# Performance work log

Measured on AMD Instinct MI355X. Metric: run time of the kernel, lower is better.

Reference implementation:

```python
import jax, jax.numpy as jnp
import numpy as np

B, N, F, U, S = 64, 4096, 2, 16, 2


def setup_inputs() -> dict:
    key = jax.random.key(0)
    ks = jax.random.split(key, 7)
    inputs = jax.random.normal(ks[0], (B, F * N), dtype=jnp.float32)
    state = jax.random.normal(ks[1], (B, U * N), dtype=jnp.float32)

    def random_walk(k):
        a = jax.random.uniform(k, (N, N), dtype=jnp.float32)
        return a / jnp.sum(a, axis=1, keepdims=True)  # row-stochastic like D^-1 A

    support0 = random_walk(ks[2])
    support1 = random_walk(ks[3])
    kshape = ((F + U) * S, U)
    scale = jnp.float32(1.0 / np.sqrt(kshape[0]))
    r_kernel = jax.random.normal(ks[4], kshape, dtype=jnp.float32) * scale
    u_kernel = jax.random.normal(ks[5], kshape, dtype=jnp.float32) * scale
    c_kernel = jax.random.normal(ks[6], kshape, dtype=jnp.float32) * scale
    return {"inputs": inputs, "state": state, "support0": support0,
            "support1": support1, "r_kernel": r_kernel, "u_kernel": u_kernel,
            "c_kernel": c_kernel}


def _diffuse(x, supports):
    # x: (B, C, N); K.dot(x, support.T)[b,c,m] = sum_n x[b,c,n] * support[m,n]
    return jnp.concatenate([jnp.einsum('bcn,mn->bcm', x, s) for s in supports], axis=1)


def reference(inputs, state, support0, support1, r_kernel, u_kernel, c_kernel):
    supports = (support0, support1)
    feats = inputs.reshape(B, F, N)
    prev = state.reshape(B, U, N)

    h = _diffuse(feats, supports).transpose(0, 2, 1)   # (B, N, S*F)
    st = _diffuse(prev, supports).transpose(0, 2, 1)   # (B, N, S*U)
    hs = jnp.concatenate([h, st], axis=-1)             # (B, N, S*(F+U))

    r = jax.nn.sigmoid(hs @ r_kernel)                  # (B, N, U)
    u = jax.nn.sigmoid(hs @ u_kernel)                  # (B, N, U)

    prev_t = prev.transpose(0, 2, 1)                   # (B, N, U)
    r_prev = (r * prev_t).transpose(0, 2, 1)           # (B, U, N)
    c_state = _diffuse(r_prev, supports).transpose(0, 2, 1)  # (B, N, S*U)
    c = jnp.tanh(jnp.concatenate([h, c_state], axis=-1) @ c_kernel)  # (B, N, U)

    z = u * prev_t + (1.0 - u) * c                     # (B, N, U)
    # original: activation=None -> linear, then K.reshape(output, (-1, units*num_nodes))
    return z.reshape(B, U * N)
```

## Files before the change

kernel.cpp:

```cpp
#include <hip/hip_runtime.h>
#include <cstdint>

#define KDIM 4096
#define NNODE 4096
#define KSPLIT 2
#define TSTEPS 128
#define THALF (TSTEPS / KSPLIT)

typedef __bf16 bf16x8 __attribute__((ext_vector_type(8)));
typedef float floatx4 __attribute__((ext_vector_type(4)));

__device__ __forceinline__ uint16_t f2b(float f) {
  union { float f; uint32_t u; } v; v.f = f;
  uint32_t u = v.u;
  return (uint16_t)((u + 0x7FFFu + ((u >> 16) & 1u)) >> 16);
}
__device__ __forceinline__ float b2f(uint16_t h) {
  union { uint32_t u; float f; } v; v.u = ((uint32_t)h) << 16; return v.f;
}
__device__ __forceinline__ uint32_t pack2(float a, float b) {
  return (uint32_t)f2b(a) | ((uint32_t)f2b(b) << 16);
}


__global__ __launch_bounds__(256) void cvt_supports(
    const float* __restrict__ s0, const float* __restrict__ s1,
    uint16_t* __restrict__ d0, uint16_t* __restrict__ d1) {
  const float* src = blockIdx.z ? s1 : s0;
  uint16_t* dst = blockIdx.z ? d1 : d0;
  const int c16 = blockIdx.x, kb = blockIdx.y;
  const int col_in = threadIdx.x >> 4, k8 = threadIdx.x & 15;
  const int col = c16 * 16 + col_in;
  const int k = kb * 128 + k8 * 8;
  const float* p = src + (size_t)col * KDIM + k;
  float4 v0 = *(const float4*)p;
  float4 v1 = *(const float4*)(p + 4);
  uint4 o;
  o.x = pack2(v0.x, v0.y); o.y = pack2(v0.z, v0.w);
  o.z = pack2(v1.x, v1.y); o.w = pack2(v1.z, v1.w);
  size_t off = ((size_t)(c16 * 128 + kb * 4 + (k8 >> 2))) * 512 +
               (size_t)((k8 & 3) * 16 + col_in) * 8;
  *(uint4*)(dst + off) = o;
}

__global__ __launch_bounds__(256) void pack_x1(
    const float* __restrict__ inp, const float* __restrict__ st,
    uint16_t* __restrict__ X1) {
  const int r16 = blockIdx.x, kb = blockIdx.y;
  const int row_in = threadIdx.x >> 4, k8 = threadIdx.x & 15;
  const int row = r16 * 16 + row_in;
  const int k = kb * 128 + k8 * 8;
  int b = row / 18, c = row - b * 18;
  const float* p = (c < 2) ? (inp + (size_t)b * 8192 + (size_t)c * 4096 + k)
                           : (st + (size_t)b * 65536 + (size_t)(c - 2) * 4096 + k);
  float4 v0 = *(const float4*)p;
  float4 v1 = *(const float4*)(p + 4);
  uint4 o;
  o.x = pack2(v0.x, v0.y); o.y = pack2(v0.z, v0.w);
  o.z = pack2(v1.x, v1.y); o.w = pack2(v1.z, v1.w);
  size_t off = ((size_t)(r16 * 128 + kb * 4 + (k8 >> 2))) * 512 +
               (size_t)((k8 & 3) * 16 + row_in) * 8;
  *(uint4*)(X1 + off) = o;
}

__device__ __forceinline__ void gl_lds16(const uint16_t* g, uint16_t* l) {
  __builtin_amdgcn_global_load_lds(
      (const __attribute__((address_space(1))) uint32_t*)g,
      (__attribute__((address_space(3))) uint32_t*)l, 16, 0, 0);
}

template <int MODE>
__global__ __launch_bounds__(256) void gemm_frag(
    const uint16_t* __restrict__ Af, const uint16_t* __restrict__ S0f,
    const uint16_t* __restrict__ S1f, uint16_t* __restrict__ D) {
  constexpr int CPB = (MODE == 1) ? 18 : 16;
  constexpr int OUTC = (MODE == 1) ? 36 : 32;
  constexpr size_t PSTRIDE = (size_t)64 * OUTC * NNODE;
  constexpr int KCH = THALF / 2;

  __shared__ uint16_t sAB[2][32][512];

  const int lane = threadIdx.x & 63, wave = threadIdx.x >> 6;
  const int wr = wave >> 1, wc = wave & 1;
  const int s = blockIdx.z & 1, ks = blockIdx.z >> 1;
  const uint16_t* __restrict__ Bf = s ? S1f : S0f;
  const int yF = blockIdx.y * 8;
  const int xF = blockIdx.x * 8;
  const int tBeg = ks * THALF;

  const bool isB = wave >= 2;
  const int half = wave & 1;
  const uint16_t* Gw = (isB ? Bf : Af) +
      ((size_t)((isB ? xF : yF) + half * 4) * 128 + (size_t)tBeg) * 512 +
      (size_t)lane * 8;
  const int slotw = (isB ? 16 : 0) + half * 8;

  floatx4 acc[4][4];
#pragma unroll
  for (int i = 0; i < 4; ++i)
#pragma unroll
    for (int j = 0; j < 4; ++j) acc[i][j] = (floatx4){0.f, 0.f, 0.f, 0.f};

  auto STAGE = [&](int bi, int c) {
    const uint16_t* gt = Gw + (size_t)c * 1024;
#pragma unroll
    for (int i = 0; i < 8; ++i) {
      const int fr = i >> 1, tt = i & 1;
      gl_lds16(gt + (size_t)fr * 65536 + (size_t)tt * 512,
               &sAB[bi][slotw + i][0]);
    }
  };

  auto COMPUTE = [&](int bi) {
#pragma unroll
    for (int tt = 0; tt < 2; ++tt) {
      bf16x8 a[4], b[4];
#pragma unroll
      for (int rt = 0; rt < 4; ++rt)
        a[rt] = *(const bf16x8*)&sAB[bi][(wr * 4 + rt) * 2 + tt][lane * 8];
#pragma unroll
      for (int ct = 0; ct < 4; ++ct)
        b[ct] = *(const bf16x8*)&sAB[bi][16 + (wc * 4 + ct) * 2 + tt][lane * 8];
#pragma unroll
      for (int rt = 0; rt < 4; ++rt)
#pragma unroll
        for (int ct = 0; ct < 4; ++ct)
          acc[rt][ct] = __builtin_amdgcn_mfma_f32_16x16x32_bf16(
              a[rt], b[ct], acc[rt][ct], 0, 0, 0);
    }
  };

  STAGE(0, 0);
  int cur = 0;
  for (int c = 0; c < KCH - 1; ++c) {
    __syncthreads();
    STAGE(cur ^ 1, c + 1);
    COMPUTE(cur);
    cur ^= 1;
  }
  __syncthreads();
  COMPUTE(cur);

  uint16_t* Dp = D + (size_t)ks * PSTRIDE;
#pragma unroll
  for (int rt = 0; rt < 4; ++rt) {
#pragma unroll
    for (int r = 0; r < 4; ++r) {
      int rowg = yF * 16 + wr * 64 + rt * 16 + (lane >> 4) * 4 + r;
      int b = rowg / CPB, c = rowg - b * CPB;
      int jj;
      if (MODE == 1) jj = (c < 2) ? (2 * s + c) : (4 + 16 * s + (c - 2));
      else jj = 16 * s + c;
      uint16_t* drow = Dp + (size_t)(b * OUTC + jj) * NNODE;
#pragma unroll
      for (int ct = 0; ct < 4; ++ct) {
        int colg = xF * 16 + wc * 64 + ct * 16 + (lane & 15);
        drow[colg] = f2b(acc[rt][ct][r]);
      }
    }
  }
}

__global__ __launch_bounds__(256) void stage2(
    const uint16_t* __restrict__ P1, const float* __restrict__ state,
    const float* __restrict__ rk, const float* __restrict__ uk,
    uint16_t* __restrict__ X2f, float* __restrict__ U) {
  constexpr size_t PS = (size_t)64 * 36 * NNODE;
  __shared__ float s_rk[576], s_uk[576];
  __shared__ uint16_t s_x2[16 * 264];
  for (int i = threadIdx.x; i < 576; i += 256) { s_rk[i] = rk[i]; s_uk[i] = uk[i]; }
  __syncthreads();
  const int b = blockIdx.x >> 4, nb = blockIdx.x & 15;
  const int i = threadIdx.x;
  const int n = nb * 256 + i;
  float hs[36];
  const uint16_t* p = P1 + (size_t)b * 36 * NNODE + n;
#pragma unroll
  for (int j = 0; j < 36; ++j)
    hs[j] = b2f(p[(size_t)j * NNODE]) + b2f(p[PS + (size_t)j * NNODE]);
  float ar[16], au[16];
#pragma unroll
  for (int k = 0; k < 16; ++k) { ar[k] = 0.f; au[k] = 0.f; }
#pragma unroll
  for (int j = 0; j < 36; ++j) {
    float h = hs[j];
#pragma unroll
    for (int k = 0; k < 16; ++k) {
      ar[k] += h * s_rk[j * 16 + k];
      au[k] += h * s_uk[j * 16 + k];
    }
  }
  const float* sp = state + (size_t)b * 65536 + n;
#pragma unroll
  for (int k = 0; k < 16; ++k) {
    float r = 1.f / (1.f + __expf(-ar[k]));
    float uu = 1.f / (1.f + __expf(-au[k]));
    float prev = sp[(size_t)k * NNODE];
    s_x2[k * 264 + i] = f2b(r * prev);
    U[(size_t)(b * 16 + k) * NNODE + n] = uu;
  }
  __syncthreads();
  uint16_t* region = X2f + ((size_t)b * 128 + nb * 8) * 512;
#pragma unroll
  for (int rr = 0; rr < 2; ++rr) {
    int fid = rr * 256 + i;
    int kk = fid & 15, qq = (fid >> 4) & 3, tl = fid >> 6;
    uint4 v = *(const uint4*)&s_x2[kk * 264 + tl * 32 + qq * 8];
    *(uint4*)(region + (size_t)fid * 8) = v;
  }
}

__global__ __launch_bounds__(256) void stage4(
    const uint16_t* __restrict__ P1, const uint16_t* __restrict__ P3,
    const float* __restrict__ U, const float* __restrict__ state,
    const float* __restrict__ ck, float* __restrict__ out) {
  constexpr size_t PS1 = (size_t)64 * 36 * NNODE;
  constexpr size_t PS3 = (size_t)64 * 32 * NNODE;
  __shared__ float s_ck[576];
  for (int i = threadIdx.x; i < 576; i += 256) s_ck[i] = ck[i];
  __syncthreads();
  int idx = blockIdx.x * 256 + threadIdx.x;
  int b = idx >> 12, n = idx & 4095;
  float hv[36];
  const uint16_t* p1 = P1 + (size_t)b * 36 * NNODE + n;
#pragma unroll
  for (int j = 0; j < 4; ++j)
    hv[j] = b2f(p1[(size_t)j * NNODE]) + b2f(p1[PS1 + (size_t)j * NNODE]);
  const uint16_t* p3 = P3 + (size_t)b * 32 * NNODE + n;
#pragma unroll
  for (int j = 0; j < 32; ++j)
    hv[4 + j] = b2f(p3[(size_t)j * NNODE]) + b2f(p3[PS3 + (size_t)j * NNODE]);
  float ac[16];
#pragma unroll
  for (int k = 0; k < 16; ++k) ac[k] = 0.f;
#pragma unroll
  for (int j = 0; j < 36; ++j) {
    float h = hv[j];
#pragma unroll
    for (int k = 0; k < 16; ++k) ac[k] += h * s_ck[j * 16 + k];
  }
  const float* sp = state + (size_t)b * 65536 + n;
  const float* up = U + (size_t)b * 16 * NNODE + n;
  float z[16];
#pragma unroll
  for (int k = 0; k < 16; ++k) {
    float e = __expf(2.f * ac[k]);
    float c = 1.f - 2.f / (e + 1.f);
    float uu = up[(size_t)k * NNODE];
    float prev = sp[(size_t)k * NNODE];
    z[k] = uu * prev + (1.f - uu) * c;
  }
  float4* po = (float4*)(out + (size_t)b * 65536 + (size_t)n * 16);
#pragma unroll
  for (int k4 = 0; k4 < 4; ++k4)
    po[k4] = make_float4(z[k4 * 4], z[k4 * 4 + 1], z[k4 * 4 + 2], z[k4 * 4 + 3]);
}

extern "C" void kernel_launch(void* const* d_in, const int* in_sizes, int n_in,
                              void* d_out, int out_size, void* d_ws, size_t ws_size,
                              hipStream_t stream) {
  const float* inputs = (const float*)d_in[0];
  const float* state = (const float*)d_in[1];
  const float* s0 = (const float*)d_in[2];
  const float* s1 = (const float*)d_in[3];
  const float* rk = (const float*)d_in[4];
  const float* uk = (const float*)d_in[5];
  const float* ck = (const float*)d_in[6];
  float* out = (float*)d_out;
  char* ws = (char*)d_ws;

  uint16_t* S0f = (uint16_t*)(ws);
  uint16_t* S1f = (uint16_t*)(ws + 33554432);
  uint16_t* X1f = (uint16_t*)(ws + 67108864);
  uint16_t* X2f = (uint16_t*)(ws + 67108864);
  uint16_t* P1 = (uint16_t*)(ws + 76546048);
  float* U = (float*)(ws + 114294784);
  uint16_t* P3 = (uint16_t*)(ws + 131072000);

  cvt_supports<<<dim3(256, 32, 2), 256, 0, stream>>>(s0, s1, S0f, S1f);
  pack_x1<<<dim3(72, 32), 256, 0, stream>>>(inputs, state, X1f);
  gemm_frag<1><<<dim3(32, 9, 2 * KSPLIT), 256, 0, stream>>>(X1f, S0f, S1f, P1);
  stage2<<<1024, 256, 0, stream>>>(P1, state, rk, uk, X2f, U);
  gemm_frag<3><<<dim3(32, 8, 2 * KSPLIT), 256, 0, stream>>>(X2f, S0f, S1f, P3);
  stage4<<<1024, 256, 0, stream>>>(P1, P3, U, state, ck, out);
}
```

Measured before the change: 386.3 us.

## Deepen GEMM LDS pipeline to four stages with partial vmcnt waits

Moves the fragment GEMM from a double-buffered loop with two k-steps per chunk to a four-slot ring of single k-step chunks, prefetching two ahead. A partial vmcnt wait and a raw s_barrier replace the full __syncthreads drain, and setprio raises MFMA priority. The aim is to keep more global-to-LDS loads in flight and overlap them better with compute. The trade-off is twice as many barriers per K and a redundant clamped reload near the tail. The correctness of the buffer reuse relies on the hand-written wait count.

```diff
diff --git a/kernel.cpp b/kernel.cpp
--- a/kernel.cpp
+++ b/kernel.cpp
@@ -76,9 +76,9 @@
   constexpr int CPB = (MODE == 1) ? 18 : 16;
   constexpr int OUTC = (MODE == 1) ? 36 : 32;
   constexpr size_t PSTRIDE = (size_t)64 * OUTC * NNODE;
-  constexpr int KCH = THALF / 2;
-
-  __shared__ uint16_t sAB[2][32][512];
+  constexpr int NCH = THALF;
+
+  __shared__ uint16_t sAB[4][16][512];
 
   const int lane = threadIdx.x & 63, wave = threadIdx.x >> 6;
   const int wr = wave >> 1, wc = wave & 1;
@@ -89,11 +89,11 @@
   const int tBeg = ks * THALF;
 
   const bool isB = wave >= 2;
-  const int half = wave & 1;
+  const int fbase = (wave & 1) * 4;
   const uint16_t* Gw = (isB ? Bf : Af) +
-      ((size_t)((isB ? xF : yF) + half * 4) * 128 + (size_t)tBeg) * 512 +
+      ((size_t)((isB ? xF : yF) + fbase) * 128 + (size_t)tBeg) * 512 +
       (size_t)lane * 8;
-  const int slotw = (isB ? 16 : 0) + half * 8;
+  const int slotw = (isB ? 8 : 0) + fbase;
 
   floatx4 acc[4][4];
 #pragma unroll
@@ -102,44 +102,40 @@
     for (int j = 0; j < 4; ++j) acc[i][j] = (floatx4){0.f, 0.f, 0.f, 0.f};
 
   auto STAGE = [&](int bi, int c) {
-    const uint16_t* gt = Gw + (size_t)c * 1024;
-#pragma unroll
-    for (int i = 0; i < 8; ++i) {
-      const int fr = i >> 1, tt = i & 1;
-      gl_lds16(gt + (size_t)fr * 65536 + (size_t)tt * 512,
-               &sAB[bi][slotw + i][0]);
-    }
+    const uint16_t* gt = Gw + (size_t)c * 512;
+#pragma unroll
+    for (int i = 0; i < 4; ++i)
+      gl_lds16(gt + (size_t)i * 65536, &sAB[bi][slotw + i][0]);
   };
 
-  auto COMPUTE = [&](int bi) {
-#pragma unroll
-    for (int tt = 0; tt < 2; ++tt) {
-      bf16x8 a[4], b[4];
-#pragma unroll
-      for (int rt = 0; rt < 4; ++rt)
-        a[rt] = *(const bf16x8*)&sAB[bi][(wr * 4 + rt) * 2 + tt][lane * 8];
+  STAGE(0, 0);
+  STAGE(1, 1);
+
+  for (int c = 0; c < NCH; ++c) {
+    int cl = c + 2; if (cl > NCH - 1) cl = NCH - 1;
+    STAGE((c + 2) & 3, cl);
+    asm volatile("s_waitcnt vmcnt(8)" ::: "memory");
+    __builtin_amdgcn_sched_barrier(0);
+    __builtin_amdgcn_s_barrier();
+    __builtin_amdgcn_sched_barrier(0);
+    const int bi = c & 3;
+    bf16x8 a[4], b[4];
+#pragma unroll
+    for (int rt = 0; rt < 4; ++rt)
+      a[rt] = *(const bf16x8*)&sAB[bi][wr * 4 + rt][lane * 8];
+#pragma unroll
+    for (int ct = 0; ct < 4; ++ct)
+      b[ct] = *(const bf16x8*)&sAB[bi][8 + wc * 4 + ct][lane * 8];
+    __builtin_amdgcn_s_setprio(1);
+#pragma unroll
+    for (int rt = 0; rt < 4; ++rt)
 #pragma unroll
       for (int ct = 0; ct < 4; ++ct)
-        b[ct] = *(const bf16x8*)&sAB[bi][16 + (wc * 4 + ct) * 2 + tt][lane * 8];
-#pragma unroll
-      for (int rt = 0; rt < 4; ++rt)
-#pragma unroll
-        for (int ct = 0; ct < 4; ++ct)
-          acc[rt][ct] = __builtin_amdgcn_mfma_f32_16x16x32_bf16(
-              a[rt], b[ct], acc[rt][ct], 0, 0, 0);
-    }
-  };
-
-  STAGE(0, 0);
-  int cur = 0;
-  for (int c = 0; c < KCH - 1; ++c) {
-    __syncthreads();
-    STAGE(cur ^ 1, c + 1);
-    COMPUTE(cur);
-    cur ^= 1;
-  }
-  __syncthreads();
-  COMPUTE(cur);
+        acc[rt][ct] = __builtin_amdgcn_mfma_f32_16x16x32_bf16(
+            a[rt], b[ct], acc[rt][ct], 0, 0, 0);
+    __builtin_amdgcn_s_setprio(0);
+    __builtin_amdgcn_sched_barrier(0);
+  }
 
   uint16_t* Dp = D + (size_t)ks * PSTRIDE;
 #pragma unroll
```

Result: faster. 365.4 us (-5.4%).
